# Optimization experiments

Hardware: AMD Instinct MI355X
Metric: run time of the kernel (lower is better)

The kernel has to match this reference:

```python
import jax, jax.numpy as jnp
import numpy as np

OUT, IN = 4096, 4096
BITS = 4
B, S = 4, 2048


def setup_inputs() -> dict:
    key = jax.random.key(0)
    k1, k2, k3, k4, k5, k6 = jax.random.split(key, 6)
    x = jax.random.normal(k1, (B, S, IN), dtype=jnp.float32)
    indices = jax.random.randint(k2, (OUT, IN), 0, 2 ** BITS, dtype=jnp.int32)
    centroids = jax.random.normal(k3, (2 ** BITS,), dtype=jnp.float32)
    # Pi stands in for the seeded rotation matrix (orthogonality not required for math check)
    Pi = jax.random.normal(k4, (IN, IN), dtype=jnp.float32) / np.sqrt(IN)
    row_norms = jax.random.uniform(k5, (OUT,), dtype=jnp.float32) + 0.5
    bias = jax.random.normal(k6, (OUT,), dtype=jnp.float32)
    return {"x": x, "indices": indices, "centroids": centroids, "Pi": Pi,
            "row_norms": row_norms, "bias": bias}


def reference(x, indices, centroids, Pi, row_norms, bias):
    # Dequantize: centroid gather -> inverse rotation -> per-row rescale
    y_hat = centroids[indices]                    # (out, in)
    W = (y_hat @ Pi) * row_norms[:, None]         # (out, in)
    # F.linear: x @ W^T + b
    return jnp.einsum('bsi,oi->bso', x, W) + bias
```

## Files before the change

kernel.cpp:

```cpp
#include <hip/hip_runtime.h>
#include <hip/hip_bf16.h>

typedef unsigned short u16;
typedef __bf16 bf16x8 __attribute__((ext_vector_type(8)));
typedef float f32x4 __attribute__((ext_vector_type(4)));


__device__ __forceinline__ u16 f32_to_bf16(float f) {
    unsigned int u = __float_as_uint(f);
    unsigned int r = (u + 0x7FFFu + ((u >> 16) & 1u)) >> 16;
    return (u16)r;
}

__device__ __forceinline__ unsigned pack2(float a, float b) {
    return (unsigned)f32_to_bf16(a) | ((unsigned)f32_to_bf16(b) << 16);
}

__device__ __forceinline__ void load_lds16(const void* g, void* s) {
    __builtin_amdgcn_global_load_lds(
        (__attribute__((address_space(1))) void*)g,
        (__attribute__((address_space(3))) void*)s,
        16, 0, 0);
}


__global__ __launch_bounds__(256) void convert_f32_bf16(
        const float* __restrict__ in, u16* __restrict__ out) {
    int i = blockIdx.x * 256 + threadIdx.x;
    const float4* in4 = (const float4*)in;
    float4 v0 = in4[(size_t)i * 2];
    float4 v1 = in4[(size_t)i * 2 + 1];
    uint4 r;
    r.x = pack2(v0.x, v0.y);
    r.y = pack2(v0.z, v0.w);
    r.z = pack2(v1.x, v1.y);
    r.w = pack2(v1.z, v1.w);
    ((uint4*)out)[i] = r;
}


__global__ __launch_bounds__(256) void dequant_kernel(
        const int* __restrict__ idx, const float* __restrict__ cent,
        u16* __restrict__ out) {
    __shared__ float lut[16];
    if (threadIdx.x < 16) lut[threadIdx.x] = cent[threadIdx.x];
    __syncthreads();
    int i = blockIdx.x * 256 + threadIdx.x;
    const int4* in4 = (const int4*)idx;
    int4 a = in4[(size_t)i * 2];
    int4 b = in4[(size_t)i * 2 + 1];
    uint4 r;
    r.x = pack2(lut[a.x], lut[a.y]);
    r.y = pack2(lut[a.z], lut[a.w]);
    r.z = pack2(lut[b.x], lut[b.y]);
    r.w = pack2(lut[b.z], lut[b.w]);
    ((uint4*)out)[i] = r;
}


__global__ __launch_bounds__(256) void transpose_to_bf16(
        const float* __restrict__ Pi, u16* __restrict__ PiT) {
    __shared__ float tile[32][33];
    const int tx = threadIdx.x;
    const int ty = threadIdx.y;
    const int j0 = blockIdx.x * 32;
    const int k0 = blockIdx.y * 32;
#pragma unroll
    for (int i = 0; i < 4; i++)
        tile[ty + 8 * i][tx] = Pi[(size_t)(k0 + ty + 8 * i) * 4096 + j0 + tx];
    __syncthreads();
#pragma unroll
    for (int i = 0; i < 4; i++)
        PiT[(size_t)(j0 + ty + 8 * i) * 4096 + k0 + tx] =
            f32_to_bf16(tile[tx][ty + 8 * i]);
}


template <int MODE>
__global__ __launch_bounds__(512, 2) void gemm_bt(
        const u16* __restrict__ A, const u16* __restrict__ Bm,
        const float* __restrict__ aux, float* __restrict__ Cf,
        u16* __restrict__ Cb, int M, int N, int K) {
    __shared__ u16 As[4 * 8192];
    __shared__ u16 Bs[4 * 8192];

    const int tid  = threadIdx.x;
    const int lane = tid & 63;
    const int wv   = tid >> 6;
    const int wr   = wv >> 2;
    const int wc   = wv & 3;

    const int nwg  = gridDim.x * gridDim.y;
    const int orig = blockIdx.y * gridDim.x + blockIdx.x;
    const int swz  = (orig & 7) * (nwg >> 3) + (orig >> 3);
    const int m0   = (swz >> 4) << 8;
    const int n0   = (swz & 15) << 8;

    const int sr  = tid >> 2;
    const int csw = ((tid & 3) ^ ((tid >> 3) & 3)) << 3;
    const u16* a0 = A  + (size_t)(m0 + sr) * K + csw;
    const u16* a1 = A  + (size_t)(m0 + 128 + sr) * K + csw;
    const u16* b0 = Bm + (size_t)(n0 + sr) * K + csw;
    const u16* b1 = Bm + (size_t)(n0 + 128 + sr) * K + csw;
    u16* dA = As + tid * 8;
    u16* dB = Bs + tid * 8;

    const int l15   = lane & 15;
    const int ck    = (((lane >> 4) ^ ((lane >> 1) & 3)) << 3);
    const int laneA = (wr * 128 + l15) * 32 + ck;
    const int laneB = (wc * 64 + l15) * 32 + ck;

    f32x4 acc[8][4];
#pragma unroll
    for (int i = 0; i < 8; i++)
#pragma unroll
        for (int j = 0; j < 4; j++) acc[i][j] = (f32x4){0.f, 0.f, 0.f, 0.f};
    bf16x8 aF[4], bF[4];

#define STAGE_A(SLOT, COL) do { \
        load_lds16(a0 + (COL), dA + (SLOT) * 8192); \
        load_lds16(a1 + (COL), dA + (SLOT) * 8192 + 4096); } while (0)
#define STAGE_B(SLOT, COL) do { \
        load_lds16(b0 + (COL), dB + (SLOT) * 8192); \
        load_lds16(b1 + (COL), dB + (SLOT) * 8192 + 4096); } while (0)
#define VMW(N) asm volatile("s_waitcnt vmcnt(" #N ")" ::: "memory")

#define SECTION(MHC, STG, RSB, RMH, RDB, VMS) do { \
        __builtin_amdgcn_s_barrier(); \
        asm volatile("s_waitcnt lgkmcnt(0)" ::: "memory"); \
        STG; \
        __builtin_amdgcn_s_setprio(1); \
        _Pragma("unroll") \
        for (int i_ = 0; i_ < 4; i_++) { \
            _Pragma("unroll") \
            for (int n_ = 0; n_ < 4; n_++) \
                acc[(MHC) * 4 + i_][n_] = __builtin_amdgcn_mfma_f32_16x16x32_bf16( \
                    aF[i_], bF[n_], acc[(MHC) * 4 + i_][n_], 0, 0, 0); \
        } \
        __builtin_amdgcn_s_setprio(0); \
        _Pragma("unroll") \
        for (int i_ = 0; i_ < 4; i_++) \
            aF[i_] = *(const bf16x8*)&As[(RSB) + laneA + ((RMH) * 4 + i_) * 512]; \
        if (RDB) { \
            _Pragma("unroll") \
            for (int i_ = 0; i_ < 4; i_++) \
                bF[i_] = *(const bf16x8*)&Bs[(RSB) + laneB + i_ * 512]; \
        } \
        VMS; \
    } while (0)

    const int NT = K >> 6;

    STAGE_A(0, 0);  STAGE_B(0, 0);
    STAGE_A(1, 32); STAGE_B(1, 32);
    STAGE_A(2, 64); STAGE_B(2, 64);
    VMW(8);
    __builtin_amdgcn_s_barrier();
#pragma unroll
    for (int i_ = 0; i_ < 4; i_++)
        aF[i_] = *(const bf16x8*)&As[laneA + i_ * 512];
#pragma unroll
    for (int i_ = 0; i_ < 4; i_++)
        bF[i_] = *(const bf16x8*)&Bs[laneB + i_ * 512];

#pragma unroll 1
    for (int t = 0; t < NT; t += 2) {
        const int cB1 = (t + 1) * 64 + 32;
        const int c2  = (t + 2 < NT) ? (t + 2) * 64 : 0;
        const int c3  = (t + 3 < NT) ? (t + 3) * 64 : 0;
        SECTION(0, STAGE_A(3, cB1),     0,     1, 0, VMW(6));
        SECTION(1, STAGE_B(3, cB1),     8192,  0, 1, (void)0);
        SECTION(0, STAGE_A(0, c2),      8192,  1, 0, VMW(6));
        SECTION(1, STAGE_B(0, c2),      16384, 0, 1, (void)0);
        SECTION(0, STAGE_A(1, c2 + 32), 16384, 1, 0, VMW(6));
        SECTION(1, STAGE_B(1, c2 + 32), 24576, 0, 1, (void)0);
        SECTION(0, STAGE_A(2, c3),      24576, 1, 0, VMW(6));
        SECTION(1, STAGE_B(2, c3),      0,     0, 1, (void)0);
    }

#undef SECTION
#undef VMW
#undef STAGE_B
#undef STAGE_A

    const int colf = l15;
    const int r0   = (lane >> 4) << 2;
#pragma unroll
    for (int m = 0; m < 8; m++) {
        const int row = m0 + wr * 128 + m * 16 + r0;
#pragma unroll
        for (int n = 0; n < 4; n++) {
            const int col = n0 + wc * 64 + n * 16 + colf;
            if (MODE == 0) {
#pragma unroll
                for (int e = 0; e < 4; e++)
                    Cb[(size_t)(row + e) * N + col] =
                        f32_to_bf16(acc[m][n][e] * aux[row + e]);
            } else {
                const float bv = aux[col];
#pragma unroll
                for (int e = 0; e < 4; e++)
                    Cf[(size_t)(row + e) * N + col] = acc[m][n][e] + bv;
            }
        }
    }
}


extern "C" void kernel_launch(void* const* d_in, const int* in_sizes, int n_in,
                              void* d_out, int out_size, void* d_ws, size_t ws_size,
                              hipStream_t stream) {
    const float* x         = (const float*)d_in[0];
    const int*   indices   = (const int*)d_in[1];
    const float* centroids = (const float*)d_in[2];
    const float* Pi        = (const float*)d_in[3];
    const float* row_norms = (const float*)d_in[4];
    const float* bias      = (const float*)d_in[5];
    float* out = (float*)d_out;

    u16* x_bf = (u16*)d_ws;
    u16* y_bf = x_bf + (size_t)33554432;
    u16* pi_t = y_bf + (size_t)16777216;
    u16* w_bf = pi_t + (size_t)16777216;

    convert_f32_bf16<<<16384, 256, 0, stream>>>(x, x_bf);
    dequant_kernel<<<8192, 256, 0, stream>>>(indices, centroids, y_bf);
    transpose_to_bf16<<<dim3(128, 128), dim3(32, 8), 0, stream>>>(Pi, pi_t);
    gemm_bt<0><<<dim3(16, 16), 512, 0, stream>>>(
        y_bf, pi_t, row_norms, nullptr, w_bf, 4096, 4096, 4096);
    gemm_bt<1><<<dim3(16, 32), 512, 0, stream>>>(
        x_bf, w_bf, bias, out, nullptr, 8192, 4096, 4096);
}
```

Baseline: 677.7 us.

## Restructure GEMM main loop into load-then-compute phases with double barriers

Result: no change. 679.6 us (+0.3%).

```diff
diff --git a/kernel.cpp b/kernel.cpp
--- a/kernel.cpp
+++ b/kernel.cpp
@@ -125,10 +125,20 @@
         load_lds16(b1 + (COL), dB + (SLOT) * 8192 + 4096); } while (0)
 #define VMW(N) asm volatile("s_waitcnt vmcnt(" #N ")" ::: "memory")
 
-#define SECTION(MHC, STG, RSB, RMH, RDB, VMS) do { \
+#define PHASE(MHC, RDB, RS, STG, VMS) do { \
+        STG; \
+        VMS; \
+        _Pragma("unroll") \
+        for (int i_ = 0; i_ < 4; i_++) \
+            aF[i_] = *(const bf16x8*)&As[(RS) + laneA + ((MHC) * 4 + i_) * 512]; \
+        if (RDB) { \
+            _Pragma("unroll") \
+            for (int i_ = 0; i_ < 4; i_++) \
+                bF[i_] = *(const bf16x8*)&Bs[(RS) + laneB + i_ * 512]; \
+        } \
         __builtin_amdgcn_s_barrier(); \
         asm volatile("s_waitcnt lgkmcnt(0)" ::: "memory"); \
-        STG; \
+        __builtin_amdgcn_sched_barrier(0); \
         __builtin_amdgcn_s_setprio(1); \
         _Pragma("unroll") \
         for (int i_ = 0; i_ < 4; i_++) { \
@@ -138,15 +148,8 @@
                     aF[i_], bF[n_], acc[(MHC) * 4 + i_][n_], 0, 0, 0); \
         } \
         __builtin_amdgcn_s_setprio(0); \
-        _Pragma("unroll") \
-        for (int i_ = 0; i_ < 4; i_++) \
-            aF[i_] = *(const bf16x8*)&As[(RSB) + laneA + ((RMH) * 4 + i_) * 512]; \
-        if (RDB) { \
-            _Pragma("unroll") \
-            for (int i_ = 0; i_ < 4; i_++) \
-                bF[i_] = *(const bf16x8*)&Bs[(RSB) + laneB + i_ * 512]; \
-        } \
-        VMS; \
+        __builtin_amdgcn_s_barrier(); \
+        asm volatile("" ::: "memory"); \
     } while (0)
 
     const int NT = K >> 6;
@@ -156,29 +159,24 @@
     STAGE_A(2, 64); STAGE_B(2, 64);
     VMW(8);
     __builtin_amdgcn_s_barrier();
-#pragma unroll
-    for (int i_ = 0; i_ < 4; i_++)
-        aF[i_] = *(const bf16x8*)&As[laneA + i_ * 512];
-#pragma unroll
-    for (int i_ = 0; i_ < 4; i_++)
-        bF[i_] = *(const bf16x8*)&Bs[laneB + i_ * 512];
+    asm volatile("" ::: "memory");
 
 #pragma unroll 1
     for (int t = 0; t < NT; t += 2) {
-        const int cB1 = (t + 1) * 64 + 32;
-        const int c2  = (t + 2 < NT) ? (t + 2) * 64 : 0;
-        const int c3  = (t + 3 < NT) ? (t + 3) * 64 : 0;
-        SECTION(0, STAGE_A(3, cB1),     0,     1, 0, VMW(6));
-        SECTION(1, STAGE_B(3, cB1),     8192,  0, 1, (void)0);
-        SECTION(0, STAGE_A(0, c2),      8192,  1, 0, VMW(6));
-        SECTION(1, STAGE_B(0, c2),      16384, 0, 1, (void)0);
-        SECTION(0, STAGE_A(1, c2 + 32), 16384, 1, 0, VMW(6));
-        SECTION(1, STAGE_B(1, c2 + 32), 24576, 0, 1, (void)0);
-        SECTION(0, STAGE_A(2, c3),      24576, 1, 0, VMW(6));
-        SECTION(1, STAGE_B(2, c3),      0,     0, 1, (void)0);
+        const int c1 = (t + 1) * 64 + 32;
+        const int c2 = (t + 2 < NT) ? (t + 2) * 64 : 0;
+        const int c3 = (t + 3 < NT) ? (t + 3) * 64 : 0;
+        PHASE(0, 1, 0,     STAGE_A(3, c1),      (void)0);
+        PHASE(1, 0, 0,     STAGE_B(3, c1),      VMW(6));
+        PHASE(0, 1, 8192,  STAGE_A(0, c2),      (void)0);
+        PHASE(1, 0, 8192,  STAGE_B(0, c2),      VMW(6));
+        PHASE(0, 1, 16384, STAGE_A(1, c2 + 32), (void)0);
+        PHASE(1, 0, 16384, STAGE_B(1, c2 + 32), VMW(6));
+        PHASE(0, 1, 24576, STAGE_A(2, c3),      (void)0);
+        PHASE(1, 0, 24576, STAGE_B(2, c3),      VMW(6));
     }
 
-#undef SECTION
+#undef PHASE
 #undef VMW
 #undef STAGE_B
 #undef STAGE_A
```
